# Kernel optimization log

Hardware: AMD Instinct MI355X
Metric: run time of the kernel (lower is better)

Reference implementation:

```python
import jax, jax.numpy as jnp
import numpy as np

# Axial permutations for num_dimensions=3, emb_dim=-1 (total rank 5), att_dims=[1,2,3]
PERMS = [[0, 2, 3, 1, 4], [0, 1, 3, 2, 4], [0, 1, 2, 3, 4]]
H_SELF = 8
H_CROSS = 8
E_HEAD = 64  # dims_embed[0] / (num_heads_self + num_heads_cross) = 1024/16


def layernorm(x, eps=1e-5):
    # nn.LayerNorm(elementwise_affine=False)
    m = x.mean(axis=-1, keepdims=True)
    v = x.var(axis=-1, keepdims=True)
    return (x - m) * jax.lax.rsqrt(v + eps)


def cross_attention(x, kv, wq, wkv, h, e):
    # x: [bb, t, d_q], kv: [bb, t_kv, d_kv]
    q = x @ wq                                   # [bb, t, h*e]
    k, v = jnp.split(kv @ wkv, 2, axis=-1)       # each [bb, t_kv, h*e]
    bb, t = q.shape[0], q.shape[1]
    tk = k.shape[1]
    q = q.reshape(bb, t, h, e)
    k = k.reshape(bb, tk, h, e)
    v = v.reshape(bb, tk, h, e)
    dots = jnp.einsum('bihe,bjhe->bhij', q, k) * (e ** -0.5)
    attn = jax.nn.softmax(dots, axis=-1)
    out = jnp.einsum('bhij,bjhe->bihe', attn, v)
    return out.reshape(bb, t, h * e)


def permute_to_from(x, kv, perm, wq, wkv, h, e):
    inv = list(np.argsort(perm))
    ax = jnp.transpose(x, perm)
    axkv = jnp.transpose(kv, perm)
    shape = list(ax.shape)
    shape_kv = list(axkv.shape)
    t, d = shape[-2], shape[-1]
    t_kv, d_kv = shape_kv[-2], shape_kv[-1]
    r1 = shape[1] / shape_kv[1]
    r2 = shape[2] / shape_kv[2]
    if int(r1) != 1:
        axkv = jnp.repeat(axkv, max(1, int(r1)), axis=1)
        ax = jnp.repeat(ax, max(1, int(1.0 / r1)), axis=1)
    if int(r2) != 1:
        axkv = jnp.repeat(axkv, max(1, int(r2)), axis=2)
        ax = jnp.repeat(ax, max(1, int(1.0 / r2)), axis=2)
    assert ax.shape[1:3] == axkv.shape[1:3]
    perm_shape = list(ax.shape)
    out = cross_attention(ax.reshape(-1, t, d), axkv.reshape(-1, t_kv, d_kv), wq, wkv, h, e)
    out = out.reshape(perm_shape[:-1] + [-1])
    if shape[1] < shape_kv[1]:  # field0 coarser along perm dim 1 -> mean-pool back
        out = out.reshape(shape[:2] + [int(1.0 / r1)] + perm_shape[2:-1] + [-1]).mean(axis=2)
    if shape[2] < shape_kv[2]:
        out = out.reshape(shape[:3] + [int(1.0 / r2)] + perm_shape[3:-1] + [-1]).mean(axis=3)
    out = out.reshape(shape[:-1] + [-1])
    return jnp.transpose(out, inv)


def setup_inputs() -> dict:
    key = jax.random.key(0)
    ks = jax.random.split(key, 8)
    B, T, LA, LO, D0, D1 = 32, 12, 12, 12, 1024, 512
    s = 0.02
    return {
        'x0': jax.random.normal(ks[0], (B, T, LA, LO, D0), dtype=jnp.float32),
        'x1': jax.random.normal(ks[1], (B, T, LA // 2, LO // 2, D1), dtype=jnp.float32),
        'wq_self': jax.random.normal(ks[2], (3, D0, 512), dtype=jnp.float32) * s,
        'wkv_self': jax.random.normal(ks[3], (3, D0, 1024), dtype=jnp.float32) * s,
        'wq_cross': jax.random.normal(ks[4], (3, D0, 512), dtype=jnp.float32) * s,
        'wkv_cross': jax.random.normal(ks[5], (3, D1, 1024), dtype=jnp.float32) * s,
        'w_out': jax.random.normal(ks[6], (3, 1024, D0), dtype=jnp.float32) * s,
        'b_out': jnp.zeros((3, D0), dtype=jnp.float32),
    }


def reference(x0, x1, wq_self, wkv_self, wq_cross, wkv_cross, w_out, b_out):
    pass_through = x0
    f0 = layernorm(x0)
    f1 = layernorm(x1)
    for ip, perm in enumerate(PERMS):
        o_self = permute_to_from(f0, f0, perm, wq_self[ip], wkv_self[ip], H_SELF, E_HEAD)
        o_cross = permute_to_from(f0, f1, perm, wq_cross[ip], wkv_cross[ip], H_CROSS, E_HEAD)
        f0 = jnp.concatenate([o_self, o_cross], axis=-1) @ w_out[ip] + b_out[ip]
    return pass_through + f0
```

## Files before the change

### kernel.cpp

```cpp
#include <hip/hip_runtime.h>
#include <hip/hip_bf16.h>


typedef __bf16 bf16x8 __attribute__((ext_vector_type(8)));
typedef float floatx4 __attribute__((ext_vector_type(4)));

#define N0 55296
#define N1 13824

#define RAW_BARRIER() asm volatile("s_barrier" ::: "memory")
#define VMCNT(n) asm volatile("s_waitcnt vmcnt(" #n ")" ::: "memory")
#define SCHED_FENCE() __builtin_amdgcn_sched_barrier(0)

__device__ __forceinline__ void gload16(const void* g, void* l) {
    __builtin_amdgcn_global_load_lds(
        (const __attribute__((address_space(1))) unsigned int*)g,
        (__attribute__((address_space(3))) unsigned int*)l, 16, 0, 0);
}

template <int SIG>
__device__ __forceinline__ int mapRow(int i) {
    if (SIG == 0) return i;
    const int b = i / 1728, r = i % 1728;
    const int d1 = r / 144, r2 = r % 144, d2 = r2 / 12, d3 = r2 % 12;
    if (SIG == 1) return b * 1728 + d3 * 144 + d1 * 12 + d2;
    if (SIG == 2) return b * 1728 + d3 * 144 + d2 * 12 + d1;
    return b * 1728 + d1 * 144 + d3 * 12 + d2;
}

template <int D>
__device__ __forceinline__ void ln_body(const float* __restrict__ xr,
                                        __hip_bfloat16* __restrict__ yr)
{
    constexpr int V = D / 256;
    const int tid = threadIdx.x;
    float vals[V];
    if constexpr (V == 4) {
        const float4 t4 = *(const float4*)(xr + tid * 4);
        vals[0] = t4.x; vals[1] = t4.y; vals[2] = t4.z; vals[3] = t4.w;
    } else {
        const float2 t2 = *(const float2*)(xr + tid * 2);
        vals[0] = t2.x; vals[1] = t2.y;
    }
    float s = 0.f, q = 0.f;
#pragma unroll
    for (int k = 0; k < V; ++k) { s += vals[k]; q += vals[k] * vals[k]; }
#pragma unroll
    for (int off = 32; off > 0; off >>= 1) {
        s += __shfl_xor(s, off);
        q += __shfl_xor(q, off);
    }
    __shared__ float rs[4], rq[4];
    const int w = tid >> 6;
    if ((tid & 63) == 0) { rs[w] = s; rq[w] = q; }
    __syncthreads();
    s = rs[0] + rs[1] + rs[2] + rs[3];
    q = rq[0] + rq[1] + rq[2] + rq[3];
    const float mean = s * (1.f / D);
    const float var  = q * (1.f / D) - mean * mean;
    const float rstd = rsqrtf(var + 1e-5f);
    __hip_bfloat16 o[V];
#pragma unroll
    for (int k = 0; k < V; ++k) o[k] = __float2bfloat16((vals[k] - mean) * rstd);
    if constexpr (V == 4) *(uint2*)(yr + tid * 4) = *(const uint2*)o;
    else                  *(uint*)(yr + tid * 2)  = *(const uint*)o;
}

__global__ __launch_bounds__(256)
void ln_all(const float* __restrict__ x0, const float* __restrict__ x1,
            __hip_bfloat16* __restrict__ f0, __hip_bfloat16* __restrict__ f1)
{
    const int row = blockIdx.x;
    if (row < N0) {
        ln_body<1024>(x0 + (size_t)row * 1024, f0 + (size_t)row * 1024);
    } else {
        const int r = row - N0;
        ln_body<512>(x1 + (size_t)r * 512, f1 + (size_t)r * 512);
    }
}

__global__ __launch_bounds__(256)
void transpose_all(const float* __restrict__ wqs, const float* __restrict__ wkvs,
                   const float* __restrict__ wqc, const float* __restrict__ wkvc,
                   const float* __restrict__ wo,
                   __hip_bfloat16* __restrict__ W1t,
                   __hip_bfloat16* __restrict__ W2t,
                   __hip_bfloat16* __restrict__ W3t)
{
    int idx = blockIdx.x;
    const float* src;
    __hip_bfloat16* dst;
    int K, N;
    if (idx < 1536) {
        const int ip = idx / 512; idx %= 512; K = 1024; N = 512;
        src = wqs + (size_t)ip * 524288;  dst = W1t + (size_t)ip * 2097152;
    } else if (idx < 4608) {
        idx -= 1536;
        const int ip = idx / 1024; idx %= 1024; K = 1024; N = 1024;
        src = wkvs + (size_t)ip * 1048576; dst = W1t + (size_t)ip * 2097152 + 524288;
    } else if (idx < 6144) {
        idx -= 4608;
        const int ip = idx / 512; idx %= 512; K = 1024; N = 512;
        src = wqc + (size_t)ip * 524288;  dst = W1t + (size_t)ip * 2097152 + 1572864;
    } else if (idx < 7680) {
        idx -= 6144;
        const int ip = idx / 512; idx %= 512; K = 512; N = 1024;
        src = wkvc + (size_t)ip * 524288; dst = W2t + (size_t)ip * 524288;
    } else {
        idx -= 7680;
        const int ip = idx / 1024; idx %= 1024; K = 1024; N = 1024;
        src = wo + (size_t)ip * 1048576;  dst = W3t + (size_t)ip * 1048576;
    }
    const int tiles_x = N >> 5;
    const int n0 = (idx % tiles_x) * 32, k0 = (idx / tiles_x) * 32;

    __shared__ float tile[32][33];
    const int tx = threadIdx.x & 31, ty = threadIdx.x >> 5;
#pragma unroll
    for (int d = 0; d < 4; ++d)
        tile[ty + d * 8][tx] = src[(size_t)(k0 + ty + d * 8) * N + n0 + tx];
    __syncthreads();
#pragma unroll
    for (int d = 0; d < 4; ++d)
        dst[(size_t)(n0 + ty + d * 8) * K + k0 + tx] = __float2bfloat16(tile[tx][ty + d * 8]);
}

__global__ __launch_bounds__(256)
void cast_w3o(const float* __restrict__ wo, __hip_bfloat16* __restrict__ W3o)
{
    const size_t i = ((size_t)blockIdx.x * 256 + threadIdx.x) * 4;
    const float4 v = *(const float4*)(wo + i);
    __hip_bfloat16 o[4] = { __float2bfloat16(v.x), __float2bfloat16(v.y),
                            __float2bfloat16(v.z), __float2bfloat16(v.w) };
    *(uint2*)(W3o + i) = *(const uint2*)o;
}

__global__ __launch_bounds__(256)
void bfold_kernel(const float* __restrict__ b_out,
                  const __hip_bfloat16* __restrict__ W1t,
                  float* __restrict__ bf)
{
    const int idx = blockIdx.x * 256 + threadIdx.x;
    const int j = idx >> 11, n = idx & 2047;
    const float* b = b_out + j * 1024;
    const __hip_bfloat16* w = W1t + ((size_t)(j + 1) * 2048 + n) * 1024;
    float s = 0.f;
#pragma unroll 4
    for (int d = 0; d < 1024; ++d) s += b[d] * __bfloat162float(w[d]);
    bf[idx] = s;
}

template <int EPI, int SIG>
__global__ __launch_bounds__(512)
void gemm8p(const __hip_bfloat16* __restrict__ A,
            const __hip_bfloat16* __restrict__ Bt,
            void* __restrict__ Cv,
            const float* __restrict__ bias,
            const float* __restrict__ resid,
            int M, int N, int K, int lda)
{
    __shared__ __align__(16) char lds[131072];

    const int gx  = gridDim.x;
    const int nwg = gx * gridDim.y;
    const int bid = blockIdx.y * gx + blockIdx.x;
    const int swz = (bid & 7) * (nwg >> 3) + (bid >> 3);
    const int m0 = (swz / gx) * 256;
    const int n0 = (swz % gx) * 256;

    const int t    = threadIdx.x;
    const int w    = t >> 6;
    const int lane = t & 63;
    const int wr   = w >> 2;
    const int wc   = w & 3;
    const int fr   = lane & 15;
    const int ksl  = lane >> 4;

    floatx4 acc[8][4] = {};

    const int tr   = t >> 3;
    const int scol = ((t & 7) ^ (tr & 7)) << 3;
    const __hip_bfloat16* aP[4];
#pragma unroll
    for (int r = 0; r < 4; ++r)
        aP[r] = A + (size_t)mapRow<SIG>(m0 + tr + r * 64) * lda + scol;
    const __hip_bfloat16* bG = Bt + (size_t)(n0 + ((tr >> 5) * 64) + (tr & 31)) * K + scol;
    const int ldst = t * 16;

    const int cg0 = ksl ^ (fr & 7);
    const int aO0 = (wr * 64 + fr) * 128 + cg0 * 16;
    const int bO0 = (wc * 32 + fr) * 128 + cg0 * 16;

    auto stageA = [&](char* buf, int h, int ka) {
        gload16(aP[h]     + ka, buf + h * 16384 + ldst);
        gload16(aP[h + 2] + ka, buf + h * 16384 + 8192 + ldst);
    };
    auto stageB = [&](char* buf, int h, int kb) {
        gload16(bG + kb + (size_t)(h * 32)       * K, buf + 32768 + h * 16384 + ldst);
        gload16(bG + kb + (size_t)(h * 32 + 128) * K, buf + 32768 + h * 16384 + 8192 + ldst);
    };

    const char* bufC = lds;
    auto ldA = [&](int h, bf16x8 (&a)[2][4]) {
#pragma unroll
        for (int mm = 0; mm < 4; ++mm) {
            a[0][mm] = *(const bf16x8*)(bufC + h * 16384 + mm * 2048 + aO0);
            a[1][mm] = *(const bf16x8*)(bufC + h * 16384 + mm * 2048 + (aO0 ^ 64));
        }
    };
    auto ldB = [&](int h, bf16x8 (&b)[2][2]) {
#pragma unroll
        for (int nn = 0; nn < 2; ++nn) {
            b[0][nn] = *(const bf16x8*)(bufC + 32768 + h * 16384 + nn * 2048 + bO0);
            b[1][nn] = *(const bf16x8*)(bufC + 32768 + h * 16384 + nn * 2048 + (bO0 ^ 64));
        }
    };
    auto quad = [&](bf16x8 (&a)[2][4], bf16x8 (&b)[2][2], int mlo, int nlo) {
        __builtin_amdgcn_s_setprio(1);
#pragma unroll
        for (int kk = 0; kk < 2; ++kk)
#pragma unroll
            for (int mm = 0; mm < 4; ++mm)
#pragma unroll
                for (int nn = 0; nn < 2; ++nn)
                    acc[mlo + mm][nlo + nn] = __builtin_amdgcn_mfma_f32_16x16x32_bf16(
                        a[kk][mm], b[kk][nn], acc[mlo + mm][nlo + nn], 0, 0, 0);
        __builtin_amdgcn_s_setprio(0);
    };

    const int NT = K >> 6;

    stageA(lds, 0, 0);
    stageB(lds, 0, 0);
    stageA(lds, 1, 0);
    stageB(lds, 1, 0);
    VMCNT(4);
    RAW_BARRIER();

    bf16x8 a0[2][4], a1[2][4], b0[2][2], b1[2][2];
    ldA(0, a0);

    for (int tt = 0; tt < NT - 1; ++tt) {
        bufC = lds + ((tt & 1) << 16);
        char* bufN = lds + (((tt + 1) & 1) << 16);
        const int kc = (tt + 1) << 6;
        ldB(0, b0);
        stageA(bufN, 0, kc);
        SCHED_FENCE();
        quad(a0, b0, 0, 0);
        VMCNT(4); RAW_BARRIER();
        ldA(1, a1);
        stageB(bufN, 0, kc);
        SCHED_FENCE();
        quad(a1, b0, 4, 0);
        VMCNT(4); RAW_BARRIER();
        ldB(1, b1);
        stageA(bufN, 1, kc);
        SCHED_FENCE();
        quad(a0, b1, 0, 2);
        VMCNT(4); RAW_BARRIER();
        bufC = bufN;
        ldA(0, a0);
        stageB(bufN, 1, kc);
        SCHED_FENCE();
        quad(a1, b1, 4, 2);
        VMCNT(4); RAW_BARRIER();
    }

    bufC = lds + (((NT - 1) & 1) << 16);
    ldB(0, b0);
    SCHED_FENCE();
    quad(a0, b0, 0, 0);
    VMCNT(2); RAW_BARRIER();
    ldA(1, a1);
    SCHED_FENCE();
    quad(a1, b0, 4, 0);
    VMCNT(0); RAW_BARRIER();
    ldB(1, b1);
    SCHED_FENCE();
    quad(a0, b1, 0, 2);
    quad(a1, b1, 4, 2);

#pragma unroll
    for (int m = 0; m < 8; ++m) {
#pragma unroll
        for (int n = 0; n < 4; ++n) {
            const int col = n0 + wc * 64 + n * 16 + fr;
#pragma unroll
            for (int r = 0; r < 4; ++r) {
                const int row = m0 + wr * 128 + m * 16 + ksl * 4 + r;
                const size_t idx = (size_t)row * N + col;
                const float v = acc[m][n][r];
                if (EPI == 0) {
                    ((__hip_bfloat16*)Cv)[idx] = __float2bfloat16(v);
                } else if (EPI == 1) {
                    ((__hip_bfloat16*)Cv)[idx] = __float2bfloat16(v + bias[col]);
                } else {
                    ((float*)Cv)[idx] = resid[idx] + v + bias[col];
                }
            }
        }
    }
}

__global__ __launch_bounds__(512)
void attn_fused(const __hip_bfloat16* __restrict__ qkv,
                const __hip_bfloat16* __restrict__ kvc,
                __hip_bfloat16* __restrict__ out, int ip)
{
    __shared__ __align__(16) __hip_bfloat16 R[12][2052];
    __shared__ __align__(16) __hip_bfloat16 KV[12][1032];
    __shared__ __hip_bfloat16 P[16][12][12];

    const int g   = blockIdx.x;
    const int tid = threadIdx.x;

    const int b  = g / 144;
    const int u1 = (g / 12) % 12;
    const int u2 = g % 12;
    int kvb, kvstride, tkc;
    if (ip == 0) {
        kvb = b * 432 + (u1 >> 1) * 6 + (u2 >> 1); kvstride = 36; tkc = 12;
    } else if (ip == 1) {
        kvb = b * 432 + u1 * 36 + (u2 >> 1); kvstride = 6; tkc = 6;
    } else {
        kvb = b * 432 + u1 * 36 + (u2 >> 1) * 6; kvstride = 1; tkc = 6;
    }

    const uint4* src = (const uint4*)(qkv + (size_t)g * 12 * 2048);
    for (int idx = tid; idx < 12 * 256; idx += 512) {
        const int row = idx >> 8, cg = idx & 255;
        *(uint4*)(&R[row][cg * 8]) = src[row * 256 + cg];
    }
    for (int idx = tid; idx < tkc * 128; idx += 512) {
        const int row = idx >> 7, cg = idx & 127;
        const uint4* kvr = (const uint4*)(kvc + (size_t)(kvb + row * kvstride) * 3072);
        *(uint4*)(&KV[row][cg * 8]) = kvr[cg];
    }
    __syncthreads();

    const int nd_self = 8 * 12 * 12;
    const int nd = nd_self + 8 * 12 * tkc;
    for (int idx = tid; idx < nd; idx += 512) {
        int h, i, j;
        const __hip_bfloat162 *q2, *k2;
        bool self = idx < nd_self;
        if (self) {
            h = idx / 144; const int rem = idx % 144; i = rem / 12; j = rem % 12;
            q2 = (const __hip_bfloat162*)(&R[i][h * 64]);
            k2 = (const __hip_bfloat162*)(&R[j][512 + h * 64]);
        } else {
            const int x = idx - nd_self;
            h = x / (12 * tkc); const int rem = x % (12 * tkc); i = rem / tkc; j = rem % tkc;
            q2 = (const __hip_bfloat162*)(&R[i][1536 + h * 64]);
            k2 = (const __hip_bfloat162*)(&KV[j][h * 64]);
        }
        float s = 0.f;
#pragma unroll
        for (int e = 0; e < 32; ++e) {
            const float2 qf = __bfloat1622float2(q2[e]);
            const float2 kf = __bfloat1622float2(k2[e]);
            s += qf.x * kf.x + qf.y * kf.y;
        }
        P[self ? h : 8 + h][i][j] = __float2bfloat16(s * 0.125f);
    }
    __syncthreads();

    if (tid < 192) {
        const int half = tid / 96, h = (tid % 96) / 12, i = tid % 12;
        const int tk = half ? tkc : 12;
        __hip_bfloat16* p = &P[half * 8 + h][i][0];
        float v[12];
        float mx = -1e30f;
        for (int j = 0; j < tk; ++j) { v[j] = __bfloat162float(p[j]); mx = fmaxf(mx, v[j]); }
        float sum = 0.f;
        for (int j = 0; j < tk; ++j) { v[j] = __expf(v[j] - mx); sum += v[j]; }
        const float inv = 1.f / sum;
        for (int j = 0; j < tk; ++j) p[j] = __float2bfloat16(v[j] * inv);
    }
    __syncthreads();

    for (int idx = tid; idx < 12 * 512; idx += 512) {
        const int i = idx >> 9, c2 = idx & 511;
        const int col = c2 * 2;
        float a0 = 0.f, a1 = 0.f;
        if (c2 < 256) {
            const int h = col >> 6;
            for (int j = 0; j < 12; ++j) {
                const float p = __bfloat162float(P[h][i][j]);
                a0 += p * __bfloat162float(R[j][1024 + col]);
                a1 += p * __bfloat162float(R[j][1024 + col + 1]);
            }
        } else {
            const int cc = col - 512;
            const int h = cc >> 6;
            for (int j = 0; j < tkc; ++j) {
                const float p = __bfloat162float(P[8 + h][i][j]);
                a0 += p * __bfloat162float(KV[j][512 + cc]);
                a1 += p * __bfloat162float(KV[j][512 + cc + 1]);
            }
        }
        __hip_bfloat16 o[2] = { __float2bfloat16(a0), __float2bfloat16(a1) };
        *(uint*)(out + (size_t)(g * 12 + i) * 1024 + col) = *(const uint*)o;
    }
}

extern "C" void kernel_launch(void* const* d_in, const int* in_sizes, int n_in,
                              void* d_out, int out_size, void* d_ws, size_t ws_size,
                              hipStream_t stream)
{
    (void)in_sizes; (void)n_in; (void)out_size; (void)ws_size;
    const float* x0        = (const float*)d_in[0];
    const float* x1        = (const float*)d_in[1];
    const float* wq_self   = (const float*)d_in[2];
    const float* wkv_self  = (const float*)d_in[3];
    const float* wq_cross  = (const float*)d_in[4];
    const float* wkv_cross = (const float*)d_in[5];
    const float* w_out     = (const float*)d_in[6];
    const float* b_out     = (const float*)d_in[7];

    __hip_bfloat16* qkv = (__hip_bfloat16*)d_out;

    char* ws = (char*)d_ws;
    size_t off = 0;
    auto alloc = [&](size_t bytes) {
        void* p = ws + off;
        off += (bytes + 255) & ~(size_t)255;
        return p;
    };
    __hip_bfloat16* f0   = (__hip_bfloat16*)alloc((size_t)N0 * 1024 * 2);
    __hip_bfloat16* f1   = (__hip_bfloat16*)alloc((size_t)N1 * 512 * 2);
    __hip_bfloat16* kvc3 = (__hip_bfloat16*)alloc((size_t)N1 * 3072 * 2);
    __hip_bfloat16* W1t  = (__hip_bfloat16*)alloc((size_t)3 * 2048 * 1024 * 2);
    __hip_bfloat16* W2t  = (__hip_bfloat16*)alloc((size_t)3 * 1024 * 512 * 2);
    __hip_bfloat16* W3t  = (__hip_bfloat16*)alloc((size_t)3 * 1024 * 1024 * 2);
    __hip_bfloat16* W3o  = (__hip_bfloat16*)alloc((size_t)2 * 1024 * 1024 * 2);
    __hip_bfloat16* Wf   = (__hip_bfloat16*)alloc((size_t)2 * 2048 * 1024 * 2);
    float*          bfo  = (float*)alloc((size_t)2 * 2048 * 4);

    ln_all<<<N0 + N1, 256, 0, stream>>>(x0, x1, f0, f1);
    transpose_all<<<10752, 256, 0, stream>>>(wq_self, wkv_self, wq_cross,
                                             wkv_cross, w_out, W1t, W2t, W3t);
    cast_w3o<<<2048, 256, 0, stream>>>(w_out, W3o);
    bfold_kernel<<<16, 256, 0, stream>>>(b_out, W1t, bfo);
    for (int j = 0; j < 2; ++j)
        gemm8p<0, 0><<<dim3(4, 8), 512, 0, stream>>>(
            W1t + (size_t)(j + 1) * 2048 * 1024, W3o + (size_t)j * 1024 * 1024,
            Wf + (size_t)j * 2048 * 1024, nullptr, nullptr, 2048, 1024, 1024, 1024);
    gemm8p<0, 0><<<dim3(12, 54), 512, 0, stream>>>(
        f1, W2t, kvc3, nullptr, nullptr, N1, 3072, 512, 512);

    gemm8p<0, 1><<<dim3(8, 216), 512, 0, stream>>>(
        f0, W1t, qkv, nullptr, nullptr, N0, 2048, 1024, 1024);
    attn_fused<<<4608, 512, 0, stream>>>(qkv, kvc3, f0, 0);

    gemm8p<1, 2><<<dim3(8, 216), 512, 0, stream>>>(
        f0, Wf, qkv, bfo, nullptr, N0, 2048, 1024, 1024);
    attn_fused<<<4608, 512, 0, stream>>>(qkv, kvc3 + 1024, f0, 1);

    gemm8p<1, 3><<<dim3(8, 216), 512, 0, stream>>>(
        f0, Wf + (size_t)2048 * 1024, qkv, bfo + 2048, nullptr, N0, 2048, 1024, 1024);
    attn_fused<<<4608, 512, 0, stream>>>(qkv, kvc3 + 2048, f0, 2);

    gemm8p<2, 0><<<dim3(4, 216), 512, 0, stream>>>(
        f0, W3t + (size_t)2 * 1024 * 1024, d_out, b_out + 2 * 1024, x0,
        N0, 1024, 1024, 1024);
}
```

Before: 1.560 ms.

## Restructure GEMM main loop into two phases and fold weight cast into transpose

The GEMM inner loop goes from four quad phases, each with its own barrier, to two phases. Each phase loads two A or B fragments from LDS and issues two staging loads before running two MFMA quads, which halves the barrier count per k-tile. The separate cast_w3o kernel is merged into transpose_all as extra blocks, saving one launch. The cost is higher register pressure from holding more fragments live, and less fine-grained overlap between global loads and compute, with different vmcnt waits.

```diff
diff --git a/kernel.cpp b/kernel.cpp
--- a/kernel.cpp
+++ b/kernel.cpp
@@ -85,9 +85,18 @@
                    const float* __restrict__ wo,
                    __hip_bfloat16* __restrict__ W1t,
                    __hip_bfloat16* __restrict__ W2t,
-                   __hip_bfloat16* __restrict__ W3t)
+                   __hip_bfloat16* __restrict__ W3t,
+                   __hip_bfloat16* __restrict__ W3o)
 {
     int idx = blockIdx.x;
+    if (idx >= 10752) {
+        const size_t i = ((size_t)(idx - 10752) * 256 + threadIdx.x) * 4;
+        const float4 v = *(const float4*)(wo + i);
+        __hip_bfloat16 o[4] = { __float2bfloat16(v.x), __float2bfloat16(v.y),
+                                __float2bfloat16(v.z), __float2bfloat16(v.w) };
+        *(uint2*)(W3o + i) = *(const uint2*)o;
+        return;
+    }
     const float* src;
     __hip_bfloat16* dst;
     int K, N;
@@ -126,16 +135,6 @@
 }
 
 __global__ __launch_bounds__(256)
-void cast_w3o(const float* __restrict__ wo, __hip_bfloat16* __restrict__ W3o)
-{
-    const size_t i = ((size_t)blockIdx.x * 256 + threadIdx.x) * 4;
-    const float4 v = *(const float4*)(wo + i);
-    __hip_bfloat16 o[4] = { __float2bfloat16(v.x), __float2bfloat16(v.y),
-                            __float2bfloat16(v.z), __float2bfloat16(v.w) };
-    *(uint2*)(W3o + i) = *(const uint2*)o;
-}
-
-__global__ __launch_bounds__(256)
 void bfold_kernel(const float* __restrict__ b_out,
                   const __hip_bfloat16* __restrict__ W1t,
                   float* __restrict__ bf)
@@ -231,49 +230,36 @@
     const int NT = K >> 6;
 
     stageA(lds, 0, 0);
+    stageA(lds, 1, 0);
     stageB(lds, 0, 0);
-    stageA(lds, 1, 0);
     stageB(lds, 1, 0);
-    VMCNT(4);
+    VMCNT(2);
     RAW_BARRIER();
 
     bf16x8 a0[2][4], a1[2][4], b0[2][2], b1[2][2];
-    ldA(0, a0);
 
     for (int tt = 0; tt < NT - 1; ++tt) {
         bufC = lds + ((tt & 1) << 16);
         char* bufN = lds + (((tt + 1) & 1) << 16);
         const int kc = (tt + 1) << 6;
-        ldB(0, b0);
-        stageA(bufN, 0, kc);
+        ldA(0, a0); ldA(1, a1); ldB(0, b0);
+        stageA(bufN, 0, kc); stageA(bufN, 1, kc);
         SCHED_FENCE();
         quad(a0, b0, 0, 0);
-        VMCNT(4); RAW_BARRIER();
-        ldA(1, a1);
-        stageB(bufN, 0, kc);
-        SCHED_FENCE();
         quad(a1, b0, 4, 0);
         VMCNT(4); RAW_BARRIER();
         ldB(1, b1);
-        stageA(bufN, 1, kc);
+        stageB(bufN, 0, kc); stageB(bufN, 1, kc);
         SCHED_FENCE();
         quad(a0, b1, 0, 2);
-        VMCNT(4); RAW_BARRIER();
-        bufC = bufN;
-        ldA(0, a0);
-        stageB(bufN, 1, kc);
-        SCHED_FENCE();
         quad(a1, b1, 4, 2);
-        VMCNT(4); RAW_BARRIER();
+        VMCNT(2); RAW_BARRIER();
     }
 
     bufC = lds + (((NT - 1) & 1) << 16);
-    ldB(0, b0);
+    ldA(0, a0); ldA(1, a1); ldB(0, b0);
     SCHED_FENCE();
     quad(a0, b0, 0, 0);
-    VMCNT(2); RAW_BARRIER();
-    ldA(1, a1);
-    SCHED_FENCE();
     quad(a1, b0, 4, 0);
     VMCNT(0); RAW_BARRIER();
     ldB(1, b1);
@@ -439,9 +425,8 @@
     float*          bfo  = (float*)alloc((size_t)2 * 2048 * 4);
 
     ln_all<<<N0 + N1, 256, 0, stream>>>(x0, x1, f0, f1);
-    transpose_all<<<10752, 256, 0, stream>>>(wq_self, wkv_self, wq_cross,
-                                             wkv_cross, w_out, W1t, W2t, W3t);
-    cast_w3o<<<2048, 256, 0, stream>>>(w_out, W3o);
+    transpose_all<<<12800, 256, 0, stream>>>(wq_self, wkv_self, wq_cross,
+                                             wkv_cross, w_out, W1t, W2t, W3t, W3o);
     bfold_kernel<<<16, 256, 0, stream>>>(b_out, W1t, bfo);
     for (int j = 0; j < 2; ++j)
         gemm8p<0, 0><<<dim3(4, 8), 512, 0, stream>>>(
```

After: 1.586 ms. No clear change (+1.7%).
